# Kernel optimization log

Hardware: AMD Instinct MI355X
Metric: run time of the kernel (lower is better)

The kernel has to match this reference:

```python
import jax, jax.numpy as jnp
import numpy as np

D = 1024
H = 16

def setup_inputs() -> dict:
    key = jax.random.key(0)
    k1, k2, k3 = jax.random.split(key, 3)
    x = jax.random.normal(k1, (2, 2048, D), dtype=jnp.float32)
    # torch Linear weights: qkv (3d, d), proj (d, d); y = x @ W.T
    w_qkv = jax.random.normal(k2, (3 * D, D), dtype=jnp.float32) * (1.0 / np.sqrt(D))
    w_proj = jax.random.normal(k3, (D, D), dtype=jnp.float32) * (1.0 / np.sqrt(D))
    return {"x": x, "w_qkv": w_qkv, "w_proj": w_proj}

def reference(x, w_qkv, w_proj):
    B, T, C = x.shape
    hd = C // H  # head dim
    qkv = x @ w_qkv.T                     # [B,T,3C]
    q, k, v = jnp.split(qkv, 3, axis=-1)
    q = q.reshape(B, T, H, hd).transpose(0, 2, 1, 3)  # [B,H,T,hd]
    k = k.reshape(B, T, H, hd).transpose(0, 2, 1, 3)
    v = v.reshape(B, T, H, hd).transpose(0, 2, 1, 3)
    att = jnp.einsum('bhqd,bhkd->bhqk', q, k) * (hd ** -0.5)  # [B,H,T,T]
    mask = jnp.triu(jnp.ones((T, T), dtype=bool), 1)
    att = jnp.where(mask, jnp.float32(-1e9), att)
    att = jax.nn.softmax(att, axis=-1)
    y = jnp.einsum('bhqk,bhkd->bhqd', att, v)  # [B,H,T,hd]
    y = y.transpose(0, 2, 1, 3).reshape(B, T, C)
    return y @ w_proj.T
```

## Files before the change

kernel.cpp:

```cpp
#include <hip/hip_runtime.h>
#include <hip/hip_bf16.h>


typedef __bf16 bf16;
typedef __bf16 bf16x8 __attribute__((ext_vector_type(8)));
typedef __bf16 bf16x4 __attribute__((ext_vector_type(4)));
typedef float f32x4 __attribute__((ext_vector_type(4)));

__device__ __forceinline__ bf16 f2bf(float f) {
    unsigned u = __builtin_bit_cast(unsigned, f);
    u += 0x7fffu + ((u >> 16) & 1u);
    unsigned short h = (unsigned short)(u >> 16);
    return __builtin_bit_cast(bf16, h);
}

__device__ __forceinline__ unsigned pack2(float a, float b) {
    unsigned ua = __builtin_bit_cast(unsigned, a);
    unsigned ub = __builtin_bit_cast(unsigned, b);
    return (ua >> 16) | (ub & 0xFFFF0000u);
}

__device__ __forceinline__ bf16x8 ld8f(const float* p) {
    f32x4 a = *(const f32x4*)p;
    f32x4 b = *(const f32x4*)(p + 4);
    bf16x8 r;
#pragma unroll
    for (int i = 0; i < 4; i++) { r[i] = f2bf(a[i]); r[i + 4] = f2bf(b[i]); }
    return r;
}

__device__ __forceinline__ void st_out(bf16* p, float v)  { *p = f2bf(v); }
__device__ __forceinline__ void st_out(float* p, float v) { *p = v; }

__global__ __launch_bounds__(256) void cvt_bf16(const float* __restrict__ src,
                                                bf16* __restrict__ dst, int n) {
    int i = (blockIdx.x * 256 + threadIdx.x) * 8;
    if (i < n) *(bf16x8*)&dst[i] = ld8f(&src[i]);
}

__device__ __forceinline__ void glds16(const bf16* g, bf16* l) {
    __builtin_amdgcn_global_load_lds(
        (const __attribute__((address_space(1))) void*)g,
        (__attribute__((address_space(3))) void*)l, 16, 0, 0);
}

template <typename TC, int BN>
__global__ __launch_bounds__(256) void gemm_glds(const bf16* __restrict__ A, int lda, int aoff,
                                                 const bf16* __restrict__ W,
                                                 TC* __restrict__ C, int N, int K) {
    constexpr int NI = (BN == 128) ? 4 : 2;
    __shared__ bf16 sA[2][128 * 32];
    __shared__ bf16 sW[2][BN * 32];
    const int bm = blockIdx.x * 128, bn = blockIdx.y * BN;
    const int tid = threadIdx.x;
    const int wave = tid >> 6, lane = tid & 63;
    const int quad = lane >> 4, l16 = lane & 15;
    const int rbase = (BN == 128) ? (wave >> 1) * 64 : wave * 32;
    const int cbase = (BN == 128) ? (wave & 1) * 64 : 0;
    const int r16 = lane >> 2, cl = lane & 3;
    const int gch = cl ^ ((r16 >> 1) & 3);
    const int sl  = (l16 >> 1) & 3;

    auto stage = [&](int bufi, int k0) {
#pragma unroll
        for (int t = 0; t < 2; t++) {
            int row = wave * 32 + t * 16 + r16;
            glds16(&A[(size_t)(bm + row) * lda + aoff + k0 + gch * 8],
                   &sA[bufi][(wave * 32 + t * 16) * 32]);
        }
        if (BN == 128) {
#pragma unroll
            for (int t = 0; t < 2; t++) {
                int row = wave * 32 + t * 16 + r16;
                glds16(&W[(size_t)(bn + row) * K + k0 + gch * 8],
                       &sW[bufi][(wave * 32 + t * 16) * 32]);
            }
        } else {
            int row = wave * 16 + r16;
            glds16(&W[(size_t)(bn + row) * K + k0 + gch * 8], &sW[bufi][(wave * 16) * 32]);
        }
    };

    f32x4 acc[NI][4] = {};

    stage(0, 0);
    asm volatile("s_waitcnt vmcnt(0)" ::: "memory");
    __syncthreads();

    const int nsteps = K >> 5;
    for (int s = 0; s < nsteps; s++) {
        const int buf = s & 1;
        if (s + 1 < nsteps) stage(buf ^ 1, (s + 1) * 32);

        bf16x8 af[NI], bfr[4];
#pragma unroll
        for (int i = 0; i < NI; i++)
            af[i] = *(bf16x8*)&sA[buf][(rbase + i * 16 + l16) * 32 + (quad ^ sl) * 8];
#pragma unroll
        for (int j = 0; j < 4; j++)
            bfr[j] = *(bf16x8*)&sW[buf][(cbase + j * 16 + l16) * 32 + (quad ^ sl) * 8];
#pragma unroll
        for (int i = 0; i < NI; i++)
#pragma unroll
            for (int j = 0; j < 4; j++)
                acc[i][j] = __builtin_amdgcn_mfma_f32_16x16x32_bf16(
                    af[i], bfr[j], acc[i][j], 0, 0, 0);

        asm volatile("s_waitcnt vmcnt(0)" ::: "memory");
        __syncthreads();
    }

#pragma unroll
    for (int i = 0; i < NI; i++)
#pragma unroll
        for (int j = 0; j < 4; j++)
#pragma unroll
            for (int r = 0; r < 4; r++) {
                int row = bm + rbase + i * 16 + quad * 4 + r;
                int col = bn + cbase + j * 16 + l16;
                st_out(&C[(size_t)row * N + col], acc[i][j][r]);
            }
}

__global__ __launch_bounds__(256) void transpose_v(const bf16* __restrict__ qkv,
                                                   bf16* __restrict__ vt) {
    __shared__ bf16 s[64][72];
    const int tt = blockIdx.x;
    const int bh = blockIdx.y;
    const int b = bh >> 4, h = bh & 15;
    const int tid = threadIdx.x;

    for (int c = tid; c < 512; c += 256) {
        int t = c >> 3, dc = (c & 7) * 8;
        *(bf16x8*)&s[t][dc] =
            *(const bf16x8*)&qkv[((size_t)(b * 2048 + tt * 64 + t)) * 3072 + 2048 + h * 64 + dc];
    }
    __syncthreads();
    for (int c = tid; c < 512; c += 256) {
        int d = c >> 3, tc = (c & 7) * 8;
        bf16x8 o;
#pragma unroll
        for (int e = 0; e < 8; e++) o[e] = s[tc + e][d];
        *(bf16x8*)&vt[((size_t)bh * 64 + d) * 2048 + tt * 64 + tc] = o;
    }
}

__global__ __launch_bounds__(128, 2) void attn(bf16* __restrict__ qkv,
                                               const bf16* __restrict__ vt) {
    const int bh = blockIdx.x;
    const int y  = blockIdx.y;
    const int g  = (y & 8) ? ((y & 16) ? (y - 24) : (y + 8)) : (31 - y);
    const int b = bh >> 4, h = bh & 15;
    const int tid  = threadIdx.x;
    const int wave = tid >> 6;
    const int lane = tid & 63;
    const int quad = lane >> 4, l16 = lane & 15;

    __shared__ bf16 sK[2][64 * 64];
    __shared__ bf16 sV[2][64 * 64];

    bf16* base = qkv + (size_t)b * 2048 * 3072;
    const bf16* vbh = vt + (size_t)bh * 64 * 2048;

    const int iq = g * 2 + wave;
    const int qb = iq * 32;
    const int kint = g;
    const float SC = 0.125f * 1.44269504f;

    const int srow = lane >> 3;
    const int schk = (lane & 7) ^ srow;

    auto stage = [&](int bufi, int kt) {
#pragma unroll
        for (int u = 0; u < 4; u++) {
            int s = wave * 4 + u;
            glds16(&base[(size_t)(kt * 64 + s * 8 + srow) * 3072 + 1024 + h * 64 + schk * 8],
                   &sK[bufi][s * 512]);
            glds16(&vbh[(size_t)(s * 8 + srow) * 2048 + kt * 64 + schk * 8],
                   &sV[bufi][s * 512]);
        }
    };

    bf16x8 qa[2][2];
#pragma unroll
    for (int rt = 0; rt < 2; rt++)
#pragma unroll
        for (int c = 0; c < 2; c++)
            qa[rt][c] = *(const bf16x8*)&base[(size_t)(qb + rt * 16 + l16) * 3072 +
                                              h * 64 + c * 32 + quad * 8];

    f32x4 acc[2][4] = {};
    float lpart[2] = {0.0f, 0.0f};
    const int sw = l16 & 7;

    auto body = [&](int kt, bool tail, int bufi) {
        const bf16* K = sK[bufi];
        const bf16* V = sV[bufi];

        bf16x8 kb[4][2];
#pragma unroll
        for (int j = 0; j < 4; j++)
#pragma unroll
            for (int c = 0; c < 2; c++)
                kb[j][c] = *(const bf16x8*)&K[(j * 16 + l16) * 64 + ((c * 4 + quad) ^ sw) * 8];

        bf16x8 vb[4][2];
#pragma unroll
        for (int dt = 0; dt < 4; dt++)
#pragma unroll
            for (int c = 0; c < 2; c++) {
                const bf16* vr = &V[(dt * 16 + l16) * 64];
                union { bf16x4 h4[2]; bf16x8 v; } u;
                u.h4[0] = *(const bf16x4*)&vr[((4 * c +     (quad >> 1)) ^ sw) * 8 + (quad & 1) * 4];
                u.h4[1] = *(const bf16x4*)&vr[((4 * c + 2 + (quad >> 1)) ^ sw) * 8 + (quad & 1) * 4];
                vb[dt][c] = u.v;
            }

        f32x4 S[2][4] = {};
#pragma unroll
        for (int j = 0; j < 4; j++)
#pragma unroll
            for (int rt = 0; rt < 2; rt++) {
                S[rt][j] = __builtin_amdgcn_mfma_f32_16x16x32_bf16(kb[j][0], qa[rt][0], S[rt][j], 0, 0, 0);
                S[rt][j] = __builtin_amdgcn_mfma_f32_16x16x32_bf16(kb[j][1], qa[rt][1], S[rt][j], 0, 0, 0);
            }

        unsigned pk[2][4][2];
#pragma unroll
        for (int rt = 0; rt < 2; rt++) {
            const int qg = qb + rt * 16 + l16;
#pragma unroll
            for (int j = 0; j < 4; j++) {
                float p[4];
#pragma unroll
                for (int r = 0; r < 4; r++) {
                    float pv = exp2f(S[rt][j][r] * SC - 8.0f);
                    if (tail) {
                        int kg = kt * 64 + j * 16 + quad * 4 + r;
                        pv = (kg > qg) ? 0.0f : pv;
                    }
                    p[r] = pv;
                }
                lpart[rt] += (p[0] + p[1]) + (p[2] + p[3]);
                pk[rt][j][0] = pack2(p[0], p[1]);
                pk[rt][j][1] = pack2(p[2], p[3]);
            }
        }

#pragma unroll
        for (int rt = 0; rt < 2; rt++)
#pragma unroll
            for (int c = 0; c < 2; c++) {
                union { unsigned u[4]; bf16x8 v; } pb;
                pb.u[0] = pk[rt][2 * c][0];
                pb.u[1] = pk[rt][2 * c][1];
                pb.u[2] = pk[rt][2 * c + 1][0];
                pb.u[3] = pk[rt][2 * c + 1][1];
#pragma unroll
                for (int dt = 0; dt < 4; dt++)
                    acc[rt][dt] = __builtin_amdgcn_mfma_f32_16x16x32_bf16(
                        vb[dt][c], pb.v, acc[rt][dt], 0, 0, 0);
            }
    };

    stage(0, 0);
    asm volatile("s_waitcnt vmcnt(0)" ::: "memory");
    __syncthreads();
    int buf = 0;
    for (int kt = 0; kt <= kint; kt++) {
        if (kt + 1 <= kint) stage(buf ^ 1, kt + 1);
        body(kt, kt == kint, buf);
        asm volatile("s_waitcnt vmcnt(0)" ::: "memory");
        __syncthreads();
        buf ^= 1;
    }

#pragma unroll
    for (int rt = 0; rt < 2; rt++) {
        lpart[rt] += __shfl_xor(lpart[rt], 16);
        lpart[rt] += __shfl_xor(lpart[rt], 32);
    }

#pragma unroll
    for (int rt = 0; rt < 2; rt++) {
        float inv = 1.0f / lpart[rt];
        int row = qb + rt * 16 + l16;
#pragma unroll
        for (int dt = 0; dt < 4; dt++) {
            bf16x4 o;
#pragma unroll
            for (int r = 0; r < 4; r++) o[r] = f2bf(acc[rt][dt][r] * inv);
            *(bf16x4*)&base[(size_t)row * 3072 + 2048 + h * 64 + dt * 16 + quad * 4] = o;
        }
    }
}

extern "C" void kernel_launch(void* const* d_in, const int* in_sizes, int n_in,
                              void* d_out, int out_size, void* d_ws, size_t ws_size,
                              hipStream_t stream) {
    (void)out_size; (void)ws_size;
    const float *x = (const float*)d_in[0], *w_qkv = (const float*)d_in[1],
                *w_proj = (const float*)d_in[2];
    for (int i = 0; i < n_in; i++) {
        if (in_sizes[i] == 4194304) x = (const float*)d_in[i];
        else if (in_sizes[i] == 3145728) w_qkv = (const float*)d_in[i];
        else if (in_sizes[i] == 1048576) w_proj = (const float*)d_in[i];
    }

    float* out = (float*)d_out;
    bf16* xb   = (bf16*)d_out;
    bf16* qkv  = (bf16*)d_ws;
    bf16* r2   = qkv + (size_t)4096 * 3072;
    bf16* wqb  = r2;
    bf16* vt   = r2;
    bf16* wpb  = r2;

    cvt_bf16<<<dim3(2048), dim3(256), 0, stream>>>(x, xb, 4096 * 1024);
    cvt_bf16<<<dim3(1536), dim3(256), 0, stream>>>(w_qkv, wqb, 3072 * 1024);
    gemm_glds<bf16, 128><<<dim3(32, 24), dim3(256), 0, stream>>>(
        xb, 1024, 0, wqb, qkv, 3072, 1024);
    transpose_v<<<dim3(32, 32), dim3(256), 0, stream>>>(qkv, vt);
    attn<<<dim3(32, 32), dim3(128), 0, stream>>>(qkv, vt);
    cvt_bf16<<<dim3(512), dim3(256), 0, stream>>>(w_proj, wpb, 1024 * 1024);
    gemm_glds<float, 128><<<dim3(32, 8), dim3(256), 0, stream>>>(
        qkv, 3072, 2048, wpb, out, 1024, 1024);
}
```

Baseline: 197.3 us.

## Split causal attention over key chunks with partial-sum combine kernel

Replaces the single attention kernel with a split-K variant. Each 256-thread block handles four query tiles and a chunk of up to eight key tiles, and writes unnormalized partial outputs and row sums to workspace. A combine kernel then sums the chunks and normalizes. This balances the triangular causal workload and raises the number of blocks in flight, at the cost of extra fp32 partial traffic and a second launch. The original kernel is kept as a fallback when the workspace is too small.

```diff
diff --git a/kernel.cpp b/kernel.cpp
--- a/kernel.cpp
+++ b/kernel.cpp
@@ -145,11 +145,25 @@
     }
 }
 
-__global__ __launch_bounds__(128, 2) void attn(bf16* __restrict__ qkv,
-                                               const bf16* __restrict__ vt) {
+
+__device__ const unsigned char d_gg[40] = {
+    0,1,2,3, 4,4, 5,5, 6,6, 7,7, 8,8,8, 9,9,9, 10,10,10, 11,11,11,
+    12,12,12,12, 13,13,13,13, 14,14,14,14, 15,15,15,15};
+__device__ const unsigned char d_cc[40] = {
+    0,0,0,0, 0,1, 0,1, 0,1, 0,1, 0,1,2, 0,1,2, 0,1,2, 0,1,2,
+    0,1,2,3, 0,1,2,3, 0,1,2,3, 0,1,2,3};
+__device__ __forceinline__ int coff_of(int gg) {
+    int q = gg >> 2, r = gg & 3;
+    return gg + 2 * q * (q - 1) + q * r;
+}
+
+__global__ __launch_bounds__(256, 2) void attn_split(bf16* __restrict__ qkv,
+                                                     const bf16* __restrict__ vt,
+                                                     float* __restrict__ partials) {
     const int bh = blockIdx.x;
-    const int y  = blockIdx.y;
-    const int g  = (y & 8) ? ((y & 16) ? (y - 24) : (y + 8)) : (31 - y);
+    const int yi = 39 - blockIdx.y;
+    const int gg = d_gg[yi];
+    const int ch = d_cc[yi];
     const int b = bh >> 4, h = bh & 15;
     const int tid  = threadIdx.x;
     const int wave = tid >> 6;
@@ -162,9 +176,13 @@
     bf16* base = qkv + (size_t)b * 2048 * 3072;
     const bf16* vbh = vt + (size_t)bh * 64 * 2048;
 
-    const int iq = g * 2 + wave;
+    const int iq = gg * 4 + wave;
     const int qb = iq * 32;
-    const int kint = g;
+    const int kint = iq >> 1;
+    const int ktmax = 2 * gg + 1;
+    const int k0 = ch * 8;
+    const int k1 = (k0 + 7 < ktmax) ? (k0 + 7) : ktmax;
+    const int nch = (gg >> 2) + 1;
     const float SC = 0.125f * 1.44269504f;
 
     const int srow = lane >> 3;
@@ -172,8 +190,8 @@
 
     auto stage = [&](int bufi, int kt) {
 #pragma unroll
-        for (int u = 0; u < 4; u++) {
-            int s = wave * 4 + u;
+        for (int u = 0; u < 2; u++) {
+            int s = wave * 2 + u;
             glds16(&base[(size_t)(kt * 64 + s * 8 + srow) * 3072 + 1024 + h * 64 + schk * 8],
                    &sK[bufi][s * 512]);
             glds16(&vbh[(size_t)(s * 8 + srow) * 2048 + kt * 64 + schk * 8],
@@ -263,6 +281,218 @@
             }
     };
 
+    stage(0, k0);
+    asm volatile("s_waitcnt vmcnt(0)" ::: "memory");
+    __syncthreads();
+    int buf = 0;
+    for (int kt = k0; kt <= k1; kt++) {
+        if (kt + 1 <= k1) stage(buf ^ 1, kt + 1);
+        if (kt <= kint) body(kt, kt == kint, buf);
+        asm volatile("s_waitcnt vmcnt(0)" ::: "memory");
+        __syncthreads();
+        buf ^= 1;
+    }
+
+    if (nch == 1) {
+#pragma unroll
+        for (int rt = 0; rt < 2; rt++) {
+            lpart[rt] += __shfl_xor(lpart[rt], 16);
+            lpart[rt] += __shfl_xor(lpart[rt], 32);
+        }
+#pragma unroll
+        for (int rt = 0; rt < 2; rt++) {
+            float inv = 1.0f / lpart[rt];
+            int row = qb + rt * 16 + l16;
+#pragma unroll
+            for (int dt = 0; dt < 4; dt++) {
+                bf16x4 o;
+#pragma unroll
+                for (int r = 0; r < 4; r++) o[r] = f2bf(acc[rt][dt][r] * inv);
+                *(bf16x4*)&base[(size_t)row * 3072 + 2048 + h * 64 + dt * 16 + quad * 4] = o;
+            }
+        }
+    } else {
+        const int sidx = (bh * 40 + coff_of(gg) + ch) * 4 + wave;
+        float* p = partials + (size_t)sidx * 2304 + lane * 36;
+#pragma unroll
+        for (int rt = 0; rt < 2; rt++)
+#pragma unroll
+            for (int dt = 0; dt < 4; dt++)
+                *(f32x4*)(p + rt * 16 + dt * 4) = acc[rt][dt];
+        p[32] = lpart[0];
+        p[33] = lpart[1];
+    }
+}
+
+__global__ __launch_bounds__(256) void attn_combine(bf16* __restrict__ qkv,
+                                                    const float* __restrict__ partials) {
+    const int bh = blockIdx.x;
+    const int gg = 4 + blockIdx.y;
+    const int b = bh >> 4, h = bh & 15;
+    const int tid  = threadIdx.x;
+    const int wave = tid >> 6;
+    const int lane = tid & 63;
+    const int quad = lane >> 4, l16 = lane & 15;
+
+    const int nch = (gg >> 2) + 1;
+    const int s0 = (bh * 40 + coff_of(gg)) * 4 + wave;
+
+    float acc[2][4][4] = {};
+    float lp[2] = {0.0f, 0.0f};
+    for (int c = 0; c < nch; c++) {
+        const float* p = partials + (size_t)(s0 + c * 4) * 2304 + lane * 36;
+#pragma unroll
+        for (int rt = 0; rt < 2; rt++)
+#pragma unroll
+            for (int dt = 0; dt < 4; dt++) {
+                f32x4 v = *(const f32x4*)(p + rt * 16 + dt * 4);
+#pragma unroll
+                for (int r = 0; r < 4; r++) acc[rt][dt][r] += v[r];
+            }
+        lp[0] += p[32];
+        lp[1] += p[33];
+    }
+
+#pragma unroll
+    for (int rt = 0; rt < 2; rt++) {
+        lp[rt] += __shfl_xor(lp[rt], 16);
+        lp[rt] += __shfl_xor(lp[rt], 32);
+    }
+
+    bf16* base = qkv + (size_t)b * 2048 * 3072;
+    const int qb = (gg * 4 + wave) * 32;
+#pragma unroll
+    for (int rt = 0; rt < 2; rt++) {
+        float inv = 1.0f / lp[rt];
+        int row = qb + rt * 16 + l16;
+#pragma unroll
+        for (int dt = 0; dt < 4; dt++) {
+            bf16x4 o;
+#pragma unroll
+            for (int r = 0; r < 4; r++) o[r] = f2bf(acc[rt][dt][r] * inv);
+            *(bf16x4*)&base[(size_t)row * 3072 + 2048 + h * 64 + dt * 16 + quad * 4] = o;
+        }
+    }
+}
+
+__global__ __launch_bounds__(128, 2) void attn2(bf16* __restrict__ qkv,
+                                                const bf16* __restrict__ vt) {
+    const int bh = blockIdx.x;
+    const int y  = blockIdx.y;
+    const int g  = (y & 8) ? ((y & 16) ? (y - 24) : (y + 8)) : (31 - y);
+    const int b = bh >> 4, h = bh & 15;
+    const int tid  = threadIdx.x;
+    const int wave = tid >> 6;
+    const int lane = tid & 63;
+    const int quad = lane >> 4, l16 = lane & 15;
+
+    __shared__ bf16 sK[2][64 * 64];
+    __shared__ bf16 sV[2][64 * 64];
+
+    bf16* base = qkv + (size_t)b * 2048 * 3072;
+    const bf16* vbh = vt + (size_t)bh * 64 * 2048;
+
+    const int iq = g * 2 + wave;
+    const int qb = iq * 32;
+    const int kint = g;
+    const float SC = 0.125f * 1.44269504f;
+
+    const int srow = lane >> 3;
+    const int schk = (lane & 7) ^ srow;
+
+    auto stage = [&](int bufi, int kt) {
+#pragma unroll
+        for (int u = 0; u < 4; u++) {
+            int s = wave * 4 + u;
+            glds16(&base[(size_t)(kt * 64 + s * 8 + srow) * 3072 + 1024 + h * 64 + schk * 8],
+                   &sK[bufi][s * 512]);
+            glds16(&vbh[(size_t)(s * 8 + srow) * 2048 + kt * 64 + schk * 8],
+                   &sV[bufi][s * 512]);
+        }
+    };
+
+    bf16x8 qa[2][2];
+#pragma unroll
+    for (int rt = 0; rt < 2; rt++)
+#pragma unroll
+        for (int c = 0; c < 2; c++)
+            qa[rt][c] = *(const bf16x8*)&base[(size_t)(qb + rt * 16 + l16) * 3072 +
+                                              h * 64 + c * 32 + quad * 8];
+
+    f32x4 acc[2][4] = {};
+    float lpart[2] = {0.0f, 0.0f};
+    const int sw = l16 & 7;
+
+    auto body = [&](int kt, bool tail, int bufi) {
+        const bf16* K = sK[bufi];
+        const bf16* V = sV[bufi];
+
+        bf16x8 kb[4][2];
+#pragma unroll
+        for (int j = 0; j < 4; j++)
+#pragma unroll
+            for (int c = 0; c < 2; c++)
+                kb[j][c] = *(const bf16x8*)&K[(j * 16 + l16) * 64 + ((c * 4 + quad) ^ sw) * 8];
+
+        bf16x8 vb[4][2];
+#pragma unroll
+        for (int dt = 0; dt < 4; dt++)
+#pragma unroll
+            for (int c = 0; c < 2; c++) {
+                const bf16* vr = &V[(dt * 16 + l16) * 64];
+                union { bf16x4 h4[2]; bf16x8 v; } u;
+                u.h4[0] = *(const bf16x4*)&vr[((4 * c +     (quad >> 1)) ^ sw) * 8 + (quad & 1) * 4];
+                u.h4[1] = *(const bf16x4*)&vr[((4 * c + 2 + (quad >> 1)) ^ sw) * 8 + (quad & 1) * 4];
+                vb[dt][c] = u.v;
+            }
+
+        f32x4 S[2][4] = {};
+#pragma unroll
+        for (int j = 0; j < 4; j++)
+#pragma unroll
+            for (int rt = 0; rt < 2; rt++) {
+                S[rt][j] = __builtin_amdgcn_mfma_f32_16x16x32_bf16(kb[j][0], qa[rt][0], S[rt][j], 0, 0, 0);
+                S[rt][j] = __builtin_amdgcn_mfma_f32_16x16x32_bf16(kb[j][1], qa[rt][1], S[rt][j], 0, 0, 0);
+            }
+
+        unsigned pk[2][4][2];
+#pragma unroll
+        for (int rt = 0; rt < 2; rt++) {
+            const int qg = qb + rt * 16 + l16;
+#pragma unroll
+            for (int j = 0; j < 4; j++) {
+                float p[4];
+#pragma unroll
+                for (int r = 0; r < 4; r++) {
+                    float pv = exp2f(S[rt][j][r] * SC - 8.0f);
+                    if (tail) {
+                        int kg = kt * 64 + j * 16 + quad * 4 + r;
+                        pv = (kg > qg) ? 0.0f : pv;
+                    }
+                    p[r] = pv;
+                }
+                lpart[rt] += (p[0] + p[1]) + (p[2] + p[3]);
+                pk[rt][j][0] = pack2(p[0], p[1]);
+                pk[rt][j][1] = pack2(p[2], p[3]);
+            }
+        }
+
+#pragma unroll
+        for (int rt = 0; rt < 2; rt++)
+#pragma unroll
+            for (int c = 0; c < 2; c++) {
+                union { unsigned u[4]; bf16x8 v; } pb;
+                pb.u[0] = pk[rt][2 * c][0];
+                pb.u[1] = pk[rt][2 * c][1];
+                pb.u[2] = pk[rt][2 * c + 1][0];
+                pb.u[3] = pk[rt][2 * c + 1][1];
+#pragma unroll
+                for (int dt = 0; dt < 4; dt++)
+                    acc[rt][dt] = __builtin_amdgcn_mfma_f32_16x16x32_bf16(
+                        vb[dt][c], pb.v, acc[rt][dt], 0, 0, 0);
+            }
+    };
+
     stage(0, 0);
     asm volatile("s_waitcnt vmcnt(0)" ::: "memory");
     __syncthreads();
@@ -298,7 +528,7 @@
 extern "C" void kernel_launch(void* const* d_in, const int* in_sizes, int n_in,
                               void* d_out, int out_size, void* d_ws, size_t ws_size,
                               hipStream_t stream) {
-    (void)out_size; (void)ws_size;
+    (void)out_size;
     const float *x = (const float*)d_in[0], *w_qkv = (const float*)d_in[1],
                 *w_proj = (const float*)d_in[2];
     for (int i = 0; i < n_in; i++) {
@@ -314,13 +544,21 @@
     bf16* wqb  = r2;
     bf16* vt   = r2;
     bf16* wpb  = r2;
+    const size_t part_off = 33554432;
+    const size_t part_need = part_off + (size_t)32 * 40 * 4 * 2304 * 4;
+    float* partials = (float*)((char*)d_ws + part_off);
 
     cvt_bf16<<<dim3(2048), dim3(256), 0, stream>>>(x, xb, 4096 * 1024);
     cvt_bf16<<<dim3(1536), dim3(256), 0, stream>>>(w_qkv, wqb, 3072 * 1024);
     gemm_glds<bf16, 128><<<dim3(32, 24), dim3(256), 0, stream>>>(
         xb, 1024, 0, wqb, qkv, 3072, 1024);
     transpose_v<<<dim3(32, 32), dim3(256), 0, stream>>>(qkv, vt);
-    attn<<<dim3(32, 32), dim3(128), 0, stream>>>(qkv, vt);
+    if (ws_size >= part_need) {
+        attn_split<<<dim3(32, 40), dim3(256), 0, stream>>>(qkv, vt, partials);
+        attn_combine<<<dim3(32, 12), dim3(256), 0, stream>>>(qkv, partials);
+    } else {
+        attn2<<<dim3(32, 32), dim3(128), 0, stream>>>(qkv, vt);
+    }
     cvt_bf16<<<dim3(512), dim3(256), 0, stream>>>(w_proj, wpb, 1024 * 1024);
     gemm_glds<float, 128><<<dim3(32, 8), dim3(256), 0, stream>>>(
         qkv, 3072, 2048, wpb, out, 1024, 1024);
```

Result: slower. 204.6 us (+3.7%).

## Fuse conversions into one kernel and write transposed V from QKV GEMM epilogue

Applied to the files above, without the earlier changes.

Merges the three fp32-to-bf16 conversion launches into a single kernel and removes the separate V transpose kernel. The QKV GEMM epilogue now writes V tiles directly in transposed layout into a dedicated workspace region. Workspace buffers are given separate offsets so the converted weights and vt no longer alias. This cuts launch count and the extra read/write pass over V, at the cost of strided bf16x4 stores in the GEMM epilogue.

```diff
diff --git a/kernel.cpp b/kernel.cpp
--- a/kernel.cpp
+++ b/kernel.cpp
@@ -32,10 +32,22 @@
 __device__ __forceinline__ void st_out(bf16* p, float v)  { *p = f2bf(v); }
 __device__ __forceinline__ void st_out(float* p, float v) { *p = v; }
 
-__global__ __launch_bounds__(256) void cvt_bf16(const float* __restrict__ src,
-                                                bf16* __restrict__ dst, int n) {
+__global__ __launch_bounds__(256) void cvt_all(const float* __restrict__ x,
+                                               const float* __restrict__ wq,
+                                               const float* __restrict__ wp,
+                                               bf16* __restrict__ xb,
+                                               bf16* __restrict__ wqb,
+                                               bf16* __restrict__ wpb) {
     int i = (blockIdx.x * 256 + threadIdx.x) * 8;
-    if (i < n) *(bf16x8*)&dst[i] = ld8f(&src[i]);
+    if (i < 4194304) {
+        *(bf16x8*)&xb[i] = ld8f(&x[i]);
+    } else if (i < 7340032) {
+        int j = i - 4194304;
+        *(bf16x8*)&wqb[j] = ld8f(&wq[j]);
+    } else {
+        int j = i - 7340032;
+        *(bf16x8*)&wpb[j] = ld8f(&wp[j]);
+    }
 }
 
 __device__ __forceinline__ void glds16(const bf16* g, bf16* l) {
@@ -44,19 +56,104 @@
         (__attribute__((address_space(3))) void*)l, 16, 0, 0);
 }
 
-template <typename TC, int BN>
-__global__ __launch_bounds__(256) void gemm_glds(const bf16* __restrict__ A, int lda, int aoff,
-                                                 const bf16* __restrict__ W,
-                                                 TC* __restrict__ C, int N, int K) {
-    constexpr int NI = (BN == 128) ? 4 : 2;
+__global__ __launch_bounds__(256) void gemm_qkv(const bf16* __restrict__ A,
+                                                const bf16* __restrict__ W,
+                                                bf16* __restrict__ C,
+                                                bf16* __restrict__ vt) {
+    constexpr int K = 1024, N = 3072;
     __shared__ bf16 sA[2][128 * 32];
-    __shared__ bf16 sW[2][BN * 32];
-    const int bm = blockIdx.x * 128, bn = blockIdx.y * BN;
+    __shared__ bf16 sW[2][128 * 32];
+    const int bm = blockIdx.x * 128, bn = blockIdx.y * 128;
     const int tid = threadIdx.x;
     const int wave = tid >> 6, lane = tid & 63;
     const int quad = lane >> 4, l16 = lane & 15;
-    const int rbase = (BN == 128) ? (wave >> 1) * 64 : wave * 32;
-    const int cbase = (BN == 128) ? (wave & 1) * 64 : 0;
+    const int rbase = (wave >> 1) * 64;
+    const int cbase = (wave & 1) * 64;
+    const int r16 = lane >> 2, cl = lane & 3;
+    const int gch = cl ^ ((r16 >> 1) & 3);
+    const int sl  = (l16 >> 1) & 3;
+
+    auto stage = [&](int bufi, int k0) {
+#pragma unroll
+        for (int t = 0; t < 2; t++) {
+            int row = wave * 32 + t * 16 + r16;
+            glds16(&A[(size_t)(bm + row) * K + k0 + gch * 8],
+                   &sA[bufi][(wave * 32 + t * 16) * 32]);
+            glds16(&W[(size_t)(bn + row) * K + k0 + gch * 8],
+                   &sW[bufi][(wave * 32 + t * 16) * 32]);
+        }
+    };
+
+    f32x4 acc[4][4] = {};
+
+    stage(0, 0);
+    asm volatile("s_waitcnt vmcnt(0)" ::: "memory");
+    __syncthreads();
+
+    for (int s = 0; s < 32; s++) {
+        const int buf = s & 1;
+        if (s + 1 < 32) stage(buf ^ 1, (s + 1) * 32);
+
+        bf16x8 af[4], bfr[4];
+#pragma unroll
+        for (int i = 0; i < 4; i++)
+            af[i] = *(bf16x8*)&sA[buf][(rbase + i * 16 + l16) * 32 + (quad ^ sl) * 8];
+#pragma unroll
+        for (int j = 0; j < 4; j++)
+            bfr[j] = *(bf16x8*)&sW[buf][(cbase + j * 16 + l16) * 32 + (quad ^ sl) * 8];
+#pragma unroll
+        for (int i = 0; i < 4; i++)
+#pragma unroll
+            for (int j = 0; j < 4; j++)
+                acc[i][j] = __builtin_amdgcn_mfma_f32_16x16x32_bf16(
+                    af[i], bfr[j], acc[i][j], 0, 0, 0);
+
+        asm volatile("s_waitcnt vmcnt(0)" ::: "memory");
+        __syncthreads();
+    }
+
+    if (bn < 2048) {
+#pragma unroll
+        for (int i = 0; i < 4; i++)
+#pragma unroll
+            for (int j = 0; j < 4; j++)
+#pragma unroll
+                for (int r = 0; r < 4; r++) {
+                    int row = bm + rbase + i * 16 + quad * 4 + r;
+                    int col = bn + cbase + j * 16 + l16;
+                    C[(size_t)row * N + col] = f2bf(acc[i][j][r]);
+                }
+    } else {
+#pragma unroll
+        for (int i = 0; i < 4; i++) {
+            int t0 = bm + rbase + i * 16 + quad * 4;
+            int bb = t0 >> 11;
+            int tl = t0 & 2047;
+#pragma unroll
+            for (int j = 0; j < 4; j++) {
+                int col = bn - 2048 + cbase + j * 16 + l16;
+                int h = col >> 6, d = col & 63;
+                bf16x4 o;
+#pragma unroll
+                for (int r = 0; r < 4; r++) o[r] = f2bf(acc[i][j][r]);
+                *(bf16x4*)&vt[((size_t)((bb * 16 + h) * 64 + d)) * 2048 + tl] = o;
+            }
+        }
+    }
+}
+
+__global__ __launch_bounds__(256) void gemm_proj(const bf16* __restrict__ A,
+                                                 const bf16* __restrict__ W,
+                                                 float* __restrict__ C) {
+    constexpr int K = 1024, N = 1024, lda = 3072, aoff = 2048;
+    __shared__ bf16 sA[2][128 * 32];
+    __shared__ bf16 sW[2][128 * 32];
+    const int bm = blockIdx.x * 128, bn = blockIdx.y * 128;
+    const int tid = threadIdx.x;
+    const int wave = tid >> 6, lane = tid & 63;
+    const int quad = lane >> 4, l16 = lane & 15;
+    const int rbase = (wave >> 1) * 64;
+    const int cbase = (wave & 1) * 64;
     const int r16 = lane >> 2, cl = lane & 3;
     const int gch = cl ^ ((r16 >> 1) & 3);
     const int sl  = (l16 >> 1) & 3;
@@ -67,40 +164,30 @@
             int row = wave * 32 + t * 16 + r16;
             glds16(&A[(size_t)(bm + row) * lda + aoff + k0 + gch * 8],
                    &sA[bufi][(wave * 32 + t * 16) * 32]);
-        }
-        if (BN == 128) {
-#pragma unroll
-            for (int t = 0; t < 2; t++) {
-                int row = wave * 32 + t * 16 + r16;
-                glds16(&W[(size_t)(bn + row) * K + k0 + gch * 8],
-                       &sW[bufi][(wave * 32 + t * 16) * 32]);
-            }
-        } else {
-            int row = wave * 16 + r16;
-            glds16(&W[(size_t)(bn + row) * K + k0 + gch * 8], &sW[bufi][(wave * 16) * 32]);
+            glds16(&W[(size_t)(bn + row) * K + k0 + gch * 8],
+                   &sW[bufi][(wave * 32 + t * 16) * 32]);
         }
     };
 
-    f32x4 acc[NI][4] = {};
+    f32x4 acc[4][4] = {};
 
     stage(0, 0);
     asm volatile("s_waitcnt vmcnt(0)" ::: "memory");
     __syncthreads();
 
-    const int nsteps = K >> 5;
-    for (int s = 0; s < nsteps; s++) {
+    for (int s = 0; s < 32; s++) {
         const int buf = s & 1;
-        if (s + 1 < nsteps) stage(buf ^ 1, (s + 1) * 32);
-
-        bf16x8 af[NI], bfr[4];
-#pragma unroll
-        for (int i = 0; i < NI; i++)
+        if (s + 1 < 32) stage(buf ^ 1, (s + 1) * 32);
+
+        bf16x8 af[4], bfr[4];
+#pragma unroll
+        for (int i = 0; i < 4; i++)
             af[i] = *(bf16x8*)&sA[buf][(rbase + i * 16 + l16) * 32 + (quad ^ sl) * 8];
 #pragma unroll
         for (int j = 0; j < 4; j++)
             bfr[j] = *(bf16x8*)&sW[buf][(cbase + j * 16 + l16) * 32 + (quad ^ sl) * 8];
 #pragma unroll
-        for (int i = 0; i < NI; i++)
+        for (int i = 0; i < 4; i++)
 #pragma unroll
             for (int j = 0; j < 4; j++)
                 acc[i][j] = __builtin_amdgcn_mfma_f32_16x16x32_bf16(
@@ -111,38 +198,15 @@
     }
 
 #pragma unroll
-    for (int i = 0; i < NI; i++)
+    for (int i = 0; i < 4; i++)
 #pragma unroll
         for (int j = 0; j < 4; j++)
 #pragma unroll
             for (int r = 0; r < 4; r++) {
                 int row = bm + rbase + i * 16 + quad * 4 + r;
                 int col = bn + cbase + j * 16 + l16;
-                st_out(&C[(size_t)row * N + col], acc[i][j][r]);
-            }
-}
-
-__global__ __launch_bounds__(256) void transpose_v(const bf16* __restrict__ qkv,
-                                                   bf16* __restrict__ vt) {
-    __shared__ bf16 s[64][72];
-    const int tt = blockIdx.x;
-    const int bh = blockIdx.y;
-    const int b = bh >> 4, h = bh & 15;
-    const int tid = threadIdx.x;
-
-    for (int c = tid; c < 512; c += 256) {
-        int t = c >> 3, dc = (c & 7) * 8;
-        *(bf16x8*)&s[t][dc] =
-            *(const bf16x8*)&qkv[((size_t)(b * 2048 + tt * 64 + t)) * 3072 + 2048 + h * 64 + dc];
-    }
-    __syncthreads();
-    for (int c = tid; c < 512; c += 256) {
-        int d = c >> 3, tc = (c & 7) * 8;
-        bf16x8 o;
-#pragma unroll
-        for (int e = 0; e < 8; e++) o[e] = s[tc + e][d];
-        *(bf16x8*)&vt[((size_t)bh * 64 + d) * 2048 + tt * 64 + tc] = o;
-    }
+                C[(size_t)row * N + col] = acc[i][j][r];
+            }
 }
 
 __global__ __launch_bounds__(128, 2) void attn(bf16* __restrict__ qkv,
@@ -309,19 +373,13 @@
 
     float* out = (float*)d_out;
     bf16* xb   = (bf16*)d_out;
-    bf16* qkv  = (bf16*)d_ws;
-    bf16* r2   = qkv + (size_t)4096 * 3072;
-    bf16* wqb  = r2;
-    bf16* vt   = r2;
-    bf16* wpb  = r2;
-
-    cvt_bf16<<<dim3(2048), dim3(256), 0, stream>>>(x, xb, 4096 * 1024);
-    cvt_bf16<<<dim3(1536), dim3(256), 0, stream>>>(w_qkv, wqb, 3072 * 1024);
-    gemm_glds<bf16, 128><<<dim3(32, 24), dim3(256), 0, stream>>>(
-        xb, 1024, 0, wqb, qkv, 3072, 1024);
-    transpose_v<<<dim3(32, 32), dim3(256), 0, stream>>>(qkv, vt);
+    bf16* qkv = (bf16*)d_ws;
+    bf16* wqb = (bf16*)((char*)d_ws + 25165824);
+    bf16* wpb = (bf16*)((char*)d_ws + 31457280);
+    bf16* vt  = (bf16*)((char*)d_ws + 33554432);
+
+    cvt_all<<<dim3(4096), dim3(256), 0, stream>>>(x, w_qkv, w_proj, xb, wqb, wpb);
+    gemm_qkv<<<dim3(32, 24), dim3(256), 0, stream>>>(xb, wqb, qkv, vt);
     attn<<<dim3(32, 32), dim3(128), 0, stream>>>(qkv, vt);
-    cvt_bf16<<<dim3(512), dim3(256), 0, stream>>>(w_proj, wpb, 1024 * 1024);
-    gemm_glds<float, 128><<<dim3(32, 8), dim3(256), 0, stream>>>(
-        qkv, 3072, 2048, wpb, out, 1024, 1024);
-}
+    gemm_proj<<<dim3(32, 8), dim3(256), 0, stream>>>(qkv, wpb, out);
+}
```

Measured after the change: 205.2 us. +4.0%, slower.

## Fuse conversions into one kernel, fold V transpose into QKV GEMM epilogue, use 128x64 tiles

Applied to the files above, without the earlier changes.

The three fp32-to-bf16 conversions now run as a single launch over separate workspace regions. The QKV GEMM epilogue writes the V columns straight into the transposed layout, so the separate transpose kernel is gone. Both GEMMs switch to 128x64 tiles, doubling the grid size, which adds parallelism but lowers per-block reuse. Launch count and an extra pass over V drop, at the cost of a larger workspace and strided 8-byte stores for V^T.

```diff
diff --git a/kernel.cpp b/kernel.cpp
--- a/kernel.cpp
+++ b/kernel.cpp
@@ -29,13 +29,22 @@
     return r;
 }
 
-__device__ __forceinline__ void st_out(bf16* p, float v)  { *p = f2bf(v); }
-__device__ __forceinline__ void st_out(float* p, float v) { *p = v; }
-
-__global__ __launch_bounds__(256) void cvt_bf16(const float* __restrict__ src,
-                                                bf16* __restrict__ dst, int n) {
+__global__ __launch_bounds__(256) void cvt_all(const float* __restrict__ x,
+                                               const float* __restrict__ wq,
+                                               const float* __restrict__ wp,
+                                               bf16* __restrict__ xb,
+                                               bf16* __restrict__ wqb,
+                                               bf16* __restrict__ wpb) {
     int i = (blockIdx.x * 256 + threadIdx.x) * 8;
-    if (i < n) *(bf16x8*)&dst[i] = ld8f(&src[i]);
+    if (i < 4194304) {
+        *(bf16x8*)&xb[i] = ld8f(&x[i]);
+    } else if (i < 7340032) {
+        int j = i - 4194304;
+        *(bf16x8*)&wqb[j] = ld8f(&wq[j]);
+    } else {
+        int j = i - 7340032;
+        *(bf16x8*)&wpb[j] = ld8f(&wp[j]);
+    }
 }
 
 __device__ __forceinline__ void glds16(const bf16* g, bf16* l) {
@@ -44,19 +53,18 @@
         (__attribute__((address_space(3))) void*)l, 16, 0, 0);
 }
 
-template <typename TC, int BN>
-__global__ __launch_bounds__(256) void gemm_glds(const bf16* __restrict__ A, int lda, int aoff,
-                                                 const bf16* __restrict__ W,
-                                                 TC* __restrict__ C, int N, int K) {
-    constexpr int NI = (BN == 128) ? 4 : 2;
+template <typename TC, bool FUSEV>
+__global__ __launch_bounds__(256) void gemm2p(const bf16* __restrict__ A, int lda, int aoff,
+                                              const bf16* __restrict__ W,
+                                              TC* __restrict__ C, int N, int K,
+                                              bf16* __restrict__ vt) {
     __shared__ bf16 sA[2][128 * 32];
-    __shared__ bf16 sW[2][BN * 32];
-    const int bm = blockIdx.x * 128, bn = blockIdx.y * BN;
+    __shared__ bf16 sW[2][64 * 32];
+    const int bm = blockIdx.x * 128, bn = blockIdx.y * 64;
     const int tid = threadIdx.x;
     const int wave = tid >> 6, lane = tid & 63;
     const int quad = lane >> 4, l16 = lane & 15;
-    const int rbase = (BN == 128) ? (wave >> 1) * 64 : wave * 32;
-    const int cbase = (BN == 128) ? (wave & 1) * 64 : 0;
+    const int rbase = wave * 32;
     const int r16 = lane >> 2, cl = lane & 3;
     const int gch = cl ^ ((r16 >> 1) & 3);
     const int sl  = (l16 >> 1) & 3;
@@ -68,20 +76,13 @@
             glds16(&A[(size_t)(bm + row) * lda + aoff + k0 + gch * 8],
                    &sA[bufi][(wave * 32 + t * 16) * 32]);
         }
-        if (BN == 128) {
-#pragma unroll
-            for (int t = 0; t < 2; t++) {
-                int row = wave * 32 + t * 16 + r16;
-                glds16(&W[(size_t)(bn + row) * K + k0 + gch * 8],
-                       &sW[bufi][(wave * 32 + t * 16) * 32]);
-            }
-        } else {
+        {
             int row = wave * 16 + r16;
             glds16(&W[(size_t)(bn + row) * K + k0 + gch * 8], &sW[bufi][(wave * 16) * 32]);
         }
     };
 
-    f32x4 acc[NI][4] = {};
+    f32x4 acc[2][4] = {};
 
     stage(0, 0);
     asm volatile("s_waitcnt vmcnt(0)" ::: "memory");
@@ -92,15 +93,15 @@
         const int buf = s & 1;
         if (s + 1 < nsteps) stage(buf ^ 1, (s + 1) * 32);
 
-        bf16x8 af[NI], bfr[4];
-#pragma unroll
-        for (int i = 0; i < NI; i++)
+        bf16x8 af[2], bfr[4];
+#pragma unroll
+        for (int i = 0; i < 2; i++)
             af[i] = *(bf16x8*)&sA[buf][(rbase + i * 16 + l16) * 32 + (quad ^ sl) * 8];
 #pragma unroll
         for (int j = 0; j < 4; j++)
-            bfr[j] = *(bf16x8*)&sW[buf][(cbase + j * 16 + l16) * 32 + (quad ^ sl) * 8];
-#pragma unroll
-        for (int i = 0; i < NI; i++)
+            bfr[j] = *(bf16x8*)&sW[buf][(j * 16 + l16) * 32 + (quad ^ sl) * 8];
+#pragma unroll
+        for (int i = 0; i < 2; i++)
 #pragma unroll
             for (int j = 0; j < 4; j++)
                 acc[i][j] = __builtin_amdgcn_mfma_f32_16x16x32_bf16(
@@ -110,38 +111,36 @@
         __syncthreads();
     }
 
-#pragma unroll
-    for (int i = 0; i < NI; i++)
-#pragma unroll
-        for (int j = 0; j < 4; j++)
-#pragma unroll
-            for (int r = 0; r < 4; r++) {
-                int row = bm + rbase + i * 16 + quad * 4 + r;
-                int col = bn + cbase + j * 16 + l16;
-                st_out(&C[(size_t)row * N + col], acc[i][j][r]);
-            }
-}
-
-__global__ __launch_bounds__(256) void transpose_v(const bf16* __restrict__ qkv,
-                                                   bf16* __restrict__ vt) {
-    __shared__ bf16 s[64][72];
-    const int tt = blockIdx.x;
-    const int bh = blockIdx.y;
-    const int b = bh >> 4, h = bh & 15;
-    const int tid = threadIdx.x;
-
-    for (int c = tid; c < 512; c += 256) {
-        int t = c >> 3, dc = (c & 7) * 8;
-        *(bf16x8*)&s[t][dc] =
-            *(const bf16x8*)&qkv[((size_t)(b * 2048 + tt * 64 + t)) * 3072 + 2048 + h * 64 + dc];
-    }
-    __syncthreads();
-    for (int c = tid; c < 512; c += 256) {
-        int d = c >> 3, tc = (c & 7) * 8;
-        bf16x8 o;
-#pragma unroll
-        for (int e = 0; e < 8; e++) o[e] = s[tc + e][d];
-        *(bf16x8*)&vt[((size_t)bh * 64 + d) * 2048 + tt * 64 + tc] = o;
+    if (!FUSEV || bn < 2048) {
+#pragma unroll
+        for (int i = 0; i < 2; i++)
+#pragma unroll
+            for (int j = 0; j < 4; j++)
+#pragma unroll
+                for (int r = 0; r < 4; r++) {
+                    int row = bm + rbase + i * 16 + quad * 4 + r;
+                    int col = bn + j * 16 + l16;
+                    if constexpr (__is_same(TC, bf16))
+                        C[(size_t)row * N + col] = f2bf(acc[i][j][r]);
+                    else
+                        C[(size_t)row * N + col] = acc[i][j][r];
+                }
+    } else {
+#pragma unroll
+        for (int i = 0; i < 2; i++) {
+            int t0 = bm + rbase + i * 16 + quad * 4;
+            int bb = t0 >> 11;
+            int tl = t0 & 2047;
+#pragma unroll
+            for (int j = 0; j < 4; j++) {
+                int col = bn - 2048 + j * 16 + l16;
+                int h = col >> 6, d = col & 63;
+                bf16x4 o;
+#pragma unroll
+                for (int r = 0; r < 4; r++) o[r] = f2bf(acc[i][j][r]);
+                *(bf16x4*)&vt[((size_t)((bb * 16 + h) * 64 + d)) * 2048 + tl] = o;
+            }
+        }
     }
 }
 
@@ -309,19 +308,15 @@
 
     float* out = (float*)d_out;
     bf16* xb   = (bf16*)d_out;
-    bf16* qkv  = (bf16*)d_ws;
-    bf16* r2   = qkv + (size_t)4096 * 3072;
-    bf16* wqb  = r2;
-    bf16* vt   = r2;
-    bf16* wpb  = r2;
-
-    cvt_bf16<<<dim3(2048), dim3(256), 0, stream>>>(x, xb, 4096 * 1024);
-    cvt_bf16<<<dim3(1536), dim3(256), 0, stream>>>(w_qkv, wqb, 3072 * 1024);
-    gemm_glds<bf16, 128><<<dim3(32, 24), dim3(256), 0, stream>>>(
-        xb, 1024, 0, wqb, qkv, 3072, 1024);
-    transpose_v<<<dim3(32, 32), dim3(256), 0, stream>>>(qkv, vt);
+    bf16* qkv = (bf16*)d_ws;
+    bf16* wqb = (bf16*)((char*)d_ws + 25165824);
+    bf16* wpb = (bf16*)((char*)d_ws + 31457280);
+    bf16* vt  = (bf16*)((char*)d_ws + 33554432);
+
+    cvt_all<<<dim3(4096), dim3(256), 0, stream>>>(x, w_qkv, w_proj, xb, wqb, wpb);
+    gemm2p<bf16, true><<<dim3(32, 48), dim3(256), 0, stream>>>(
+        xb, 1024, 0, wqb, qkv, 3072, 1024, vt);
     attn<<<dim3(32, 32), dim3(128), 0, stream>>>(qkv, vt);
-    cvt_bf16<<<dim3(512), dim3(256), 0, stream>>>(w_proj, wpb, 1024 * 1024);
-    gemm_glds<float, 128><<<dim3(32, 8), dim3(256), 0, stream>>>(
-        qkv, 3072, 2048, wpb, out, 1024, 1024);
-}
+    gemm2p<float, false><<<dim3(32, 16), dim3(256), 0, stream>>>(
+        qkv, 3072, 2048, wpb, out, 1024, 1024, nullptr);
+}
```

Measured after the change: 192.4 us. 1.03x faster.
